# Performance work log

Measured on AMD Instinct MI355X. Metric: run time of the kernel, lower is better.

The kernel has to match this reference:

```python
import jax, jax.numpy as jnp
import numpy as np

N = 200_000      # nodes
E = 6_400_000    # edges (avg degree 32)
G = 2_000        # graphs
SD = 10          # state_dim
ROUNDS = 3


def setup_inputs() -> dict:
    key = jax.random.key(0)
    ks = jax.random.split(key, 10)
    node_coordinates = jax.random.normal(ks[0], (N, 3), dtype=jnp.float32)
    node_graph_index = jnp.sort(jax.random.randint(ks[1], (N,), 0, G))
    node_from = jax.random.randint(ks[2], (E,), 0, N)
    node_to = jax.random.randint(ks[3], (E,), 0, N)
    edge_lengths = jax.random.uniform(ks[4], (E, 1), dtype=jnp.float32)
    edge_vectors = jax.random.normal(ks[5], (E, 3), dtype=jnp.float32)
    # message net: Linear(14 -> 10), torch default uniform init
    lim = 1.0 / np.sqrt(SD + 4)
    W_msg = jax.random.uniform(ks[6], (SD + 4, SD), minval=-lim, maxval=lim, dtype=jnp.float32)
    b_msg = jax.random.uniform(ks[7], (SD,), minval=-lim, maxval=lim, dtype=jnp.float32)
    # output net: Linear(10 -> 4), xavier_normal weight, default bias
    W_out = jax.random.normal(ks[8], (SD, 4), dtype=jnp.float32) * np.float32(np.sqrt(2.0 / (SD + 4)))
    lim_o = 1.0 / np.sqrt(SD)
    b_out = jax.random.uniform(ks[9], (4,), minval=-lim_o, maxval=lim_o, dtype=jnp.float32)
    return dict(node_coordinates=node_coordinates, edge_lengths=edge_lengths,
                edge_vectors=edge_vectors, W_msg=W_msg, b_msg=b_msg,
                W_out=W_out, b_out=b_out, node_from=node_from, node_to=node_to,
                node_graph_index=node_graph_index, num_nodes=N, num_graphs=G)


def reference(node_coordinates, edge_lengths, edge_vectors, W_msg, b_msg,
              W_out, b_out, node_from, node_to, node_graph_index,
              num_nodes, num_graphs):
    c_from = node_coordinates[node_from]                      # (E,3) gather
    c_to = node_coordinates[node_to]                          # (E,3) gather
    coord_sum = jnp.sum(jnp.abs(c_from), axis=1, keepdims=True)       # (E,1)
    dot1 = jnp.sum(c_from * c_to, axis=1, keepdims=True)              # (E,1)
    dot2 = jnp.sum(c_from * edge_vectors, axis=1, keepdims=True)      # (E,1)
    geo = jnp.concatenate([edge_lengths, coord_sum, dot1, dot2], axis=1)  # (E,4), identical every round

    state = jnp.zeros((num_nodes, SD), dtype=node_coordinates.dtype)
    for _ in range(ROUNDS):
        inp = jnp.concatenate([state[node_from], geo], axis=1)        # (E,14)
        msg = jnp.tanh(inp @ W_msg + b_msg)                           # (E,10)
        state = state + jax.ops.segment_sum(msg, node_to, num_segments=num_nodes)

    graph_state = jax.ops.segment_sum(state, node_graph_index, num_segments=num_graphs)  # (G,10)
    ev = graph_state @ W_out + b_out                                  # (G,4)
    gamma, v, alpha, beta = jnp.split(ev, 4, axis=1)
    sp = jax.nn.softplus
    return jnp.concatenate([gamma, sp(v), sp(alpha) + 1.0, sp(beta)], axis=1)
```

## Files before the change

kernel.cpp:

```cpp
#include <hip/hip_runtime.h>
#include <hip/hip_fp16.h>
#include <math.h>

#define SD 10
#define BSZ 64
#define EB 512
#define CTHR 1024
#define BINB 10
#define NBIN_MAX 256

typedef unsigned uvec4 __attribute__((ext_vector_type(4)));
struct rec12 { unsigned x, y, z; };
union U32H2 { unsigned u; __half2 h; };

__device__ __forceinline__ float tanh_fast(float x) {
    float e = __expf(2.0f * x);
    float r = __builtin_amdgcn_rcpf(1.0f + e);
    return 1.0f - 2.0f * r;
}

__device__ __forceinline__ float softplus_f(float x) {
    return fmaxf(x, 0.0f) + log1pf(expf(-fabsf(x)));
}


__global__ __launch_bounds__(256) void coords4_kernel(
    const float* __restrict__ coords, float4* __restrict__ coords4, int N)
{
    int n = blockIdx.x * blockDim.x + threadIdx.x;
    if (n >= N) return;
    float4 c;
    c.x = coords[n * 3 + 0];
    c.y = coords[n * 3 + 1];
    c.z = coords[n * 3 + 2];
    c.w = fabsf(c.x) + fabsf(c.y) + fabsf(c.z);
    coords4[n] = c;
}


__global__ __launch_bounds__(CTHR) void pass1_kernel(
    const float* __restrict__ elen,
    const float* __restrict__ evec,
    const int* __restrict__ nfrom,
    const int* __restrict__ nto,
    unsigned* __restrict__ s1addr,
    rec12* __restrict__ payA,
    int E, int NBIN)
{
    __shared__ unsigned hbin[NBIN_MAX];
    __shared__ unsigned curbin[NBIN_MAX];
    int b = blockIdx.x, t = threadIdx.x;
    long long ebeg = (long long)E * b / EB;
    long long eend = (long long)E * (b + 1) / EB;

    if (t < NBIN_MAX) hbin[t] = 0;
    __syncthreads();
    for (long long e = ebeg + t; e < eend; e += CTHR)
        atomicAdd(&hbin[((unsigned)__builtin_nontemporal_load(&nto[e])) >> BINB], 1u);
    __syncthreads();
    {
        unsigned v = (t < NBIN_MAX) ? hbin[t] : 0u;
        for (int d = 1; d < NBIN_MAX; d <<= 1) {
            unsigned x = (t < NBIN_MAX && t >= d) ? hbin[t - d] : 0u;
            __syncthreads();
            if (t < NBIN_MAX) hbin[t] += x;
            __syncthreads();
        }
        if (t < NBIN_MAX) curbin[t] = (unsigned)ebeg + hbin[t] - v;
    }
    __syncthreads();
    if (t < NBIN) s1addr[(size_t)t * EB + b] = curbin[t];
    if (t == 0)  s1addr[(size_t)NBIN * EB + b] = (unsigned)eend;
    __syncthreads();

    for (long long e = ebeg + t; e < eend; e += CTHR) {
        int nf = __builtin_nontemporal_load(&nfrom[e]);
        int nt = __builtin_nontemporal_load(&nto[e]);
        float l  = __builtin_nontemporal_load(&elen[e]);
        float ex = __builtin_nontemporal_load(&evec[e * 3 + 0]);
        float ey = __builtin_nontemporal_load(&evec[e * 3 + 1]);
        float ez = __builtin_nontemporal_load(&evec[e * 3 + 2]);
        unsigned bin = ((unsigned)nt) >> BINB;
        unsigned pos = atomicAdd(&curbin[bin], 1u);
        U32H2 a, c;
        a.h = __floats2half2_rn(l, ex);
        c.h = __floats2half2_rn(ey, ez);
        rec12 r;
        r.x = (unsigned)nf | (((unsigned)nt & ((1u << BINB) - 1u)) << 18);
        r.y = a.u;
        r.z = c.u;
        payA[pos] = r;
    }
}

__global__ __launch_bounds__(256) void colsum_kernel(
    const unsigned* __restrict__ s1addr, unsigned* __restrict__ binsum)
{
    __shared__ unsigned red[256];
    int q = blockIdx.x, t = threadIdx.x;
    red[t] = s1addr[(size_t)q * EB + t] + s1addr[(size_t)q * EB + t + 256];
    __syncthreads();
    for (int d = 128; d > 0; d >>= 1) {
        if (t < d) red[t] += red[t + d];
        __syncthreads();
    }
    if (t == 0) binsum[q] = red[0];
}

__global__ __launch_bounds__(256) void binstart_kernel(
    const unsigned* __restrict__ binsum, unsigned* __restrict__ binstart,
    unsigned* __restrict__ nodestart, int NBIN, int E)
{
    int t = threadIdx.x;
    unsigned b0 = binsum[0];
    for (int q = t; q <= NBIN; q += 256) binstart[q] = binsum[q] - b0;
    if (t == 0) nodestart[(size_t)NBIN << BINB] = (unsigned)E;
}

__global__ __launch_bounds__(CTHR) void pass2_kernel(
    const unsigned* __restrict__ s1addr,
    const unsigned* __restrict__ binstart,
    const float4* __restrict__ coords4,
    const rec12* __restrict__ src,
    rec12* __restrict__ dst,
    unsigned* __restrict__ nodestart,
    int NBIN)
{
    __shared__ unsigned segst[EB];
    __shared__ unsigned spref[EB + 1];
    __shared__ unsigned hist[1 << BINB];
    __shared__ unsigned cur[1 << BINB];
    int q = blockIdx.x, t = threadIdx.x;

    if (t < EB) {
        unsigned st = s1addr[(size_t)q * EB + t];
        unsigned en = s1addr[(size_t)(q + 1) * EB + t];
        segst[t] = st;
        spref[t] = en - st;
    }
    hist[t] = 0;
    __syncthreads();
    {
        unsigned v = (t < EB) ? spref[t] : 0u;
        for (int d = 1; d < EB; d <<= 1) {
            unsigned x = (t < EB && t >= d) ? spref[t - d] : 0u;
            __syncthreads();
            if (t < EB) spref[t] += x;
            __syncthreads();
        }
        unsigned incl = (t < EB) ? spref[t] : 0u;
        __syncthreads();
        if (t < EB) spref[t] = incl - v;
        if (t == EB - 1) spref[EB] = incl;
    }
    __syncthreads();
    unsigned len = spref[EB];
    unsigned obase = binstart[q];
    const unsigned* srcw = (const unsigned*)src;

    for (unsigned i = t; i < len; i += CTHR) {
        unsigned lo = 0, hi = EB;
#pragma unroll
        for (int s = 0; s < 9; s++) {
            unsigned mid = (lo + hi) >> 1;
            if (spref[mid] <= i) lo = mid; else hi = mid;
        }
        unsigned x0 = srcw[(size_t)(segst[lo] + (i - spref[lo])) * 3];
        atomicAdd(&hist[(x0 >> 18) & ((1u << BINB) - 1u)], 1u);
    }
    __syncthreads();
    unsigned hv = hist[t];
    __syncthreads();
    for (int d = 1; d < (1 << BINB); d <<= 1) {
        unsigned x = (t >= d) ? hist[t - d] : 0u;
        __syncthreads();
        hist[t] += x;
        __syncthreads();
    }
    unsigned excl = hist[t] - hv;
    cur[t] = obase + excl;
    nodestart[((size_t)q << BINB) + t] = obase + excl;
    __syncthreads();

    rec12 p0; float4 cf0;
    {
        unsigned i0 = t;
        if (i0 < len) {
            unsigned lo = 0, hi = EB;
#pragma unroll
            for (int s = 0; s < 9; s++) {
                unsigned mid = (lo + hi) >> 1;
                if (spref[mid] <= i0) lo = mid; else hi = mid;
            }
            p0 = src[segst[lo] + (i0 - spref[lo])];
            cf0 = coords4[p0.x & 0x3FFFFu];
        }
    }
    for (unsigned i = t; i < len; i += CTHR) {
        unsigned i1 = i + CTHR;
        rec12 p1 = p0; float4 cf1 = cf0;
        if (i1 < len) {
            unsigned lo = 0, hi = EB;
#pragma unroll
            for (int s = 0; s < 9; s++) {
                unsigned mid = (lo + hi) >> 1;
                if (spref[mid] <= i1) lo = mid; else hi = mid;
            }
            p1 = src[segst[lo] + (i1 - spref[lo])];
            cf1 = coords4[p1.x & 0x3FFFFu];
        }
        unsigned key = (p0.x >> 18) & ((1u << BINB) - 1u);
        unsigned pos = atomicAdd(&cur[key], 1u);
        unsigned nt = ((unsigned)q << BINB) | key;
        float4 ct = coords4[nt];
        U32H2 ya, za;
        ya.u = p0.y; za.u = p0.z;
        float g0 = __low2float(ya.h), ev0 = __high2float(ya.h);
        float ev1 = __low2float(za.h), ev2 = __high2float(za.h);
        float g2 = cf0.x * ct.x + cf0.y * ct.y + cf0.z * ct.z;
        float g3 = cf0.x * ev0 + cf0.y * ev1 + cf0.z * ev2;
        U32H2 oy, oz;
        oy.h = __floats2half2_rn(g0, cf0.w);
        oz.h = __floats2half2_rn(g2, g3);
        rec12 r;
        r.x = (p0.x & 0x3FFFFu) | ((nt & (BSZ - 1u)) << 18);
        r.y = oy.u;
        r.z = oz.u;
        dst[pos] = r;
        p0 = p1; cf0 = cf1;
    }
}


__global__ __launch_bounds__(256) void wstate_kernel(
    const float* __restrict__ state, const float* __restrict__ Wm,
    const float* __restrict__ bm, __half* __restrict__ wsth, int N)
{
    int n = blockIdx.x * blockDim.x + threadIdx.x;
    if (n >= N) return;
    const float2* sp = (const float2*)(state + (size_t)n * SD);
    float s[SD];
#pragma unroll
    for (int h = 0; h < 5; h++) { float2 v = sp[h]; s[2*h] = v.x; s[2*h+1] = v.y; }
    float t[SD];
#pragma unroll
    for (int j = 0; j < SD; j++) t[j] = bm[j];
#pragma unroll
    for (int k = 0; k < SD; k++) {
#pragma unroll
        for (int j = 0; j < SD; j++) t[j] += s[k] * Wm[k * SD + j];
    }
    unsigned* dp = (unsigned*)(wsth + (size_t)n * SD);
#pragma unroll
    for (int h = 0; h < 5; h++) {
        U32H2 cv;
        cv.h = __floats2half2_rn(t[2*h], t[2*h+1]);
        dp[h] = cv.u;
    }
}

template <bool FIRST>
__global__ __launch_bounds__(256) void round_run_kernel(
    const unsigned* __restrict__ nodestart,
    const rec12* __restrict__ payload,
    const float* __restrict__ Wm,
    const float* __restrict__ bm,
    const __half* __restrict__ wsth,
    const float* __restrict__ state_prev,
    float* __restrict__ state_next,
    int N, int E)
{
    __shared__ float acc[BSZ * SD];
    int k = blockIdx.x;
    for (int i = threadIdx.x; i < BSZ * SD; i += 256) acc[i] = 0.0f;

    int lane = threadIdx.x & 63;
    int wv = threadIdx.x >> 6;
    int grp0 = lane / 10;
    bool active = grp0 < 6;
    int grp = active ? grp0 : 5;
    int j = active ? (lane - grp0 * 10) : (lane - 60);

    float w0 = Wm[10 * SD + j];
    float w1 = Wm[11 * SD + j];
    float w2 = Wm[12 * SD + j];
    float w3 = Wm[13 * SD + j];
    float bb = bm[j];
    __syncthreads();

    unsigned beg = nodestart[(size_t)k << 6];
    unsigned end = nodestart[(size_t)(k + 1) << 6];
    unsigned len = end - beg;
    unsigned Q = (len + 3) >> 2;
    unsigned rbeg = beg + (unsigned)wv * Q;
    unsigned rend = rbeg + Q; if (rend > end) rend = end;
    unsigned eclamp = (unsigned)E - 1u;

    unsigned e0 = rbeg + (unsigned)grp;
    rec12 P0 = payload[e0 <= eclamp ? e0 : eclamp];
    unsigned e1 = e0 + 6;
    rec12 P1 = payload[e1 <= eclamp ? e1 : eclamp];
    float T0 = bb, T1 = bb;
    if (!FIRST) T0 = __half2float(wsth[(size_t)(P0.x & 0x3FFFFu) * SD + j]);

    int cur_lnt = -1;
    float accv = 0.0f;

    for (unsigned base = rbeg; base < rend; base += 6) {
        unsigned e2 = base + 12 + (unsigned)grp;
        rec12 P2 = payload[e2 <= eclamp ? e2 : eclamp];
        if (!FIRST) T1 = __half2float(wsth[(size_t)(P1.x & 0x3FFFFu) * SD + j]);
        unsigned e = base + (unsigned)grp;
        if (active && e < rend) {
            int lnt = (int)((P0.x >> 18) & (BSZ - 1));
            U32H2 c01, c23;
            c01.u = P0.y; c23.u = P0.z;
            float g0 = __low2float(c01.h), g1 = __high2float(c01.h);
            float g2 = __low2float(c23.h), g3 = __high2float(c23.h);
            float t = T0 + g0 * w0 + g1 * w1 + g2 * w2 + g3 * w3;
            if (lnt != cur_lnt) {
                if (cur_lnt >= 0) atomicAdd(&acc[cur_lnt * SD + j], accv);
                accv = 0.0f;
                cur_lnt = lnt;
            }
            accv += tanh_fast(t);
        }
        P0 = P1; P1 = P2; T0 = T1;
    }
    if (active && cur_lnt >= 0) atomicAdd(&acc[cur_lnt * SD + j], accv);
    __syncthreads();

    int base_o = k * BSZ * SD;
    int lim = N * SD - base_o;
    for (int i = threadIdx.x; i < BSZ * SD; i += 256) {
        if (i < lim) {
            float v = acc[i];
            if (!FIRST) v += state_prev[base_o + i];
            state_next[base_o + i] = v;
        }
    }
}


__global__ __launch_bounds__(256) void goff_kernel(
    const int* __restrict__ gidx, unsigned* __restrict__ goff, int N, int G)
{
    int n = blockIdx.x * blockDim.x + threadIdx.x;
    if (n >= N) return;
    int g = gidx[n];
    if (n == 0) {
        for (int q = 0; q <= g; q++) goff[q] = 0;
    } else {
        int gp = gidx[n - 1];
        for (int q = gp + 1; q <= g; q++) goff[q] = (unsigned)n;
    }
    if (n == N - 1) {
        for (int q = g + 1; q <= G; q++) goff[q] = (unsigned)N;
    }
}

__global__ __launch_bounds__(256) void gsum_kernel(
    const float* __restrict__ state, const unsigned* __restrict__ goff,
    float* __restrict__ gstate, int G)
{
    int tid = blockIdx.x * blockDim.x + threadIdx.x;
    if (tid >= G * SD * 4) return;
    int s = tid & 3;
    int rest = tid >> 2;
    int g = rest / SD;
    int j = rest - g * SD;
    unsigned beg = goff[g], end = goff[g + 1];
    unsigned len = end - beg;
    unsigned b0 = beg + (len * (unsigned)s) / 4u;
    unsigned b1 = beg + (len * (unsigned)(s + 1)) / 4u;
    float a = 0.0f;
    for (unsigned n = b0; n < b1; n++) a += state[(size_t)n * SD + j];
    atomicAdd(&gstate[(size_t)g * SD + j], a);
}

__global__ __launch_bounds__(256) void out_kernel(
    const float* __restrict__ gstate, const float* __restrict__ Wo,
    const float* __restrict__ bo, float* __restrict__ out, int G)
{
    int g = blockIdx.x * blockDim.x + threadIdx.x;
    if (g >= G) return;
    float s[SD];
#pragma unroll
    for (int k = 0; k < SD; k++) s[k] = gstate[(size_t)g * SD + k];
    float ev[4];
#pragma unroll
    for (int c = 0; c < 4; c++) {
        float a = bo[c];
#pragma unroll
        for (int k = 0; k < SD; k++) a += s[k] * Wo[k * 4 + c];
        ev[c] = a;
    }
    out[g * 4 + 0] = ev[0];
    out[g * 4 + 1] = softplus_f(ev[1]);
    out[g * 4 + 2] = softplus_f(ev[2]) + 1.0f;
    out[g * 4 + 3] = softplus_f(ev[3]);
}


template <bool FIRST>
__global__ __launch_bounds__(256) void edge_kernel_fb(
    const float* __restrict__ coords, const float* __restrict__ elen,
    const float* __restrict__ evec, const float* __restrict__ Wm,
    const float* __restrict__ bm, const int* __restrict__ nfrom,
    const int* __restrict__ nto, const float* __restrict__ state_prev,
    float* __restrict__ state_next, int E)
{
    int e = blockIdx.x * blockDim.x + threadIdx.x;
    if (e >= E) return;
    int nf = nfrom[e];
    int nt = nto[e];
    float cf0 = coords[nf*3+0], cf1 = coords[nf*3+1], cf2 = coords[nf*3+2];
    float ct0 = coords[nt*3+0], ct1 = coords[nt*3+1], ct2 = coords[nt*3+2];
    float ev0 = evec[e*3+0], ev1 = evec[e*3+1], ev2 = evec[e*3+2];
    float g0 = elen[e];
    float g1 = fabsf(cf0) + fabsf(cf1) + fabsf(cf2);
    float g2 = cf0*ct0 + cf1*ct1 + cf2*ct2;
    float g3 = cf0*ev0 + cf1*ev1 + cf2*ev2;
    float acc[SD];
#pragma unroll
    for (int j = 0; j < SD; j++) {
        acc[j] = bm[j] + g0*Wm[10*SD+j] + g1*Wm[11*SD+j] + g2*Wm[12*SD+j] + g3*Wm[13*SD+j];
    }
    if (!FIRST) {
        const float2* sp = (const float2*)(state_prev + (size_t)nf * SD);
        float s[SD];
#pragma unroll
        for (int h = 0; h < 5; h++) { float2 v = sp[h]; s[2*h] = v.x; s[2*h+1] = v.y; }
#pragma unroll
        for (int k = 0; k < SD; k++) {
#pragma unroll
            for (int j = 0; j < SD; j++) acc[j] += s[k] * Wm[k*SD+j];
        }
    }
    float* dst = state_next + (size_t)nt * SD;
#pragma unroll
    for (int j = 0; j < SD; j++) atomicAdd(dst + j, tanh_fast(acc[j]));
}

__global__ __launch_bounds__(256) void graph_reduce_fb(
    const float* __restrict__ state, const int* __restrict__ gidx,
    float* __restrict__ gstate, int N)
{
    int n = blockIdx.x * blockDim.x + threadIdx.x;
    if (n >= N) return;
    int g = gidx[n];
    const float2* sp = (const float2*)(state + (size_t)n * SD);
    float* dst = gstate + (size_t)g * SD;
#pragma unroll
    for (int h = 0; h < 5; h++) {
        float2 v = sp[h];
        atomicAdd(dst + 2*h, v.x);
        atomicAdd(dst + 2*h + 1, v.y);
    }
}


extern "C" void kernel_launch(void* const* d_in, const int* in_sizes, int n_in,
                              void* d_out, int out_size, void* d_ws, size_t ws_size,
                              hipStream_t stream) {
    const float* coords = (const float*)d_in[0];
    const float* elen   = (const float*)d_in[1];
    const float* evec   = (const float*)d_in[2];
    const float* Wm     = (const float*)d_in[3];
    const float* bm     = (const float*)d_in[4];
    const float* Wo     = (const float*)d_in[5];
    const float* bo     = (const float*)d_in[6];
    const int* nfrom    = (const int*)d_in[7];
    const int* nto      = (const int*)d_in[8];
    const int* gidx     = (const int*)d_in[9];

    const int E = in_sizes[1];
    const int N = in_sizes[9];
    const int G = out_size / 4;

    const int NBIN = (N + (1 << BINB) - 1) >> BINB;
    const int NB   = (N + BSZ - 1) / BSZ;

    const int BLK = 256;
    const int ng = (N + BLK - 1) / BLK;
    const int gg = (G + BLK - 1) / BLK;

    auto align256 = [](size_t x) { return (x + 255) & ~(size_t)255; };
    const size_t state_bytes = align256((size_t)N * SD * sizeof(float));
    const size_t wst_bytes   = align256((size_t)N * SD * sizeof(__half) + 256);
    const size_t payA_bytes  = align256((size_t)E * sizeof(rec12) + 256);
    const size_t payB_bytes  = align256((size_t)E * sizeof(rec12) + 256);
    const size_t s1a_bytes   = align256((size_t)(NBIN_MAX + 1) * EB * sizeof(unsigned));
    const size_t bsum_bytes  = align256((size_t)(NBIN_MAX + 1) * sizeof(unsigned));
    const size_t nst_bytes   = align256(((size_t)NBIN_MAX * (1 << BINB) + 2) * sizeof(unsigned));
    const size_t goff_bytes  = align256((size_t)(G + 1) * sizeof(unsigned));
    const size_t gst_bytes   = align256((size_t)G * SD * sizeof(float));
    const size_t c4_bytes    = align256((size_t)N * sizeof(float4));

    size_t o = 0;
    char* w = (char*)d_ws;
    float* stateA      = (float*)(w + o);    o += state_bytes;
    float* stateB      = (float*)(w + o);    o += state_bytes;
    __half* wsth       = (__half*)(w + o);   o += wst_bytes;
    rec12* payA        = (rec12*)(w + o);    o += payA_bytes;
    rec12* payB        = (rec12*)(w + o);    o += payB_bytes;
    unsigned* s1addr   = (unsigned*)(w + o); o += s1a_bytes;
    unsigned* binsum   = (unsigned*)(w + o); o += bsum_bytes;
    unsigned* binstart = (unsigned*)(w + o); o += bsum_bytes;
    unsigned* nodestart= (unsigned*)(w + o); o += nst_bytes;
    unsigned* goff     = (unsigned*)(w + o); o += goff_bytes;
    float* gstate      = (float*)(w + o);    o += gst_bytes;
    float4* coords4    = (float4*)(w + o);   o += c4_bytes;

    if (o <= ws_size && NBIN <= NBIN_MAX && N < (1 << 18)) {
        coords4_kernel<<<ng, BLK, 0, stream>>>(coords, coords4, N);
        pass1_kernel<<<EB, CTHR, 0, stream>>>(elen, evec, nfrom, nto,
                                              s1addr, payA, E, NBIN);
        colsum_kernel<<<NBIN + 1, 256, 0, stream>>>(s1addr, binsum);
        binstart_kernel<<<1, 256, 0, stream>>>(binsum, binstart, nodestart, NBIN, E);
        pass2_kernel<<<NBIN, CTHR, 0, stream>>>(s1addr, binstart, coords4,
                                                payA, payB, nodestart, NBIN);
        round_run_kernel<true><<<NB, BLK, 0, stream>>>(nodestart, payB, Wm, bm,
                                                       wsth, stateB, stateA, N, E);
        wstate_kernel<<<ng, BLK, 0, stream>>>(stateA, Wm, bm, wsth, N);
        round_run_kernel<false><<<NB, BLK, 0, stream>>>(nodestart, payB, Wm, bm,
                                                        wsth, stateA, stateB, N, E);
        wstate_kernel<<<ng, BLK, 0, stream>>>(stateB, Wm, bm, wsth, N);
        round_run_kernel<false><<<NB, BLK, 0, stream>>>(nodestart, payB, Wm, bm,
                                                        wsth, stateB, stateA, N, E);
        hipMemsetAsync(gstate, 0, (size_t)G * SD * sizeof(float), stream);
        goff_kernel<<<ng, BLK, 0, stream>>>(gidx, goff, N, G);
        gsum_kernel<<<(G * SD * 4 + BLK - 1) / BLK, BLK, 0, stream>>>(stateA, goff, gstate, G);
        out_kernel<<<gg, BLK, 0, stream>>>(gstate, Wo, bo, (float*)d_out, G);
    } else {
        const int eg = (E + BLK - 1) / BLK;
        float* gstateF = (float*)(w + 2 * state_bytes);
        hipMemsetAsync(stateA, 0, state_bytes, stream);
        hipMemsetAsync(gstateF, 0, (size_t)G * SD * sizeof(float), stream);
        edge_kernel_fb<true><<<eg, BLK, 0, stream>>>(coords, elen, evec, Wm, bm,
                                                     nfrom, nto, stateA, stateA, E);
        hipMemcpyAsync(stateB, stateA, state_bytes, hipMemcpyDeviceToDevice, stream);
        edge_kernel_fb<false><<<eg, BLK, 0, stream>>>(coords, elen, evec, Wm, bm,
                                                      nfrom, nto, stateA, stateB, E);
        hipMemcpyAsync(stateA, stateB, state_bytes, hipMemcpyDeviceToDevice, stream);
        edge_kernel_fb<false><<<eg, BLK, 0, stream>>>(coords, elen, evec, Wm, bm,
                                                      nfrom, nto, stateB, stateA, E);
        graph_reduce_fb<<<ng, BLK, 0, stream>>>(stateA, gidx, gstateF, N);
        out_kernel<<<gg, BLK, 0, stream>>>(gstateF, Wo, bo, (float*)d_out, G);
    }
}
```

Before: 702.3 us.

## Stage pass2 scatter through LDS per key half-range for coalesced output writes

Bins are reduced from 10 to 9 bits, so each bin covers fewer nodes and more bins exist. Pass2 now sweeps the input once per half of the key range and scatters matching records into a large shared-memory staging buffer (about 130 KB of LDS). It then computes the geometry features and writes the output contiguously instead of scattering each record to global memory. The cost is re-reading the bin's input once per key half, a large LDS footprint that limits occupancy, and an unstaged fallback path when a half-range overflows the buffer.

```diff
diff --git a/kernel.cpp b/kernel.cpp
--- a/kernel.cpp
+++ b/kernel.cpp
@@ -6,8 +6,10 @@
 #define BSZ 64
 #define EB 512
 #define CTHR 1024
-#define BINB 10
-#define NBIN_MAX 256
+#define BINB 9
+#define NBIN_MAX 512
+#define HSZ 256
+#define SCAP 10880
 
 typedef unsigned uvec4 __attribute__((ext_vector_type(4)));
 struct rec12 { unsigned x, y, z; };
@@ -130,7 +132,9 @@
     __shared__ unsigned spref[EB + 1];
     __shared__ unsigned hist[1 << BINB];
     __shared__ unsigned cur[1 << BINB];
+    __shared__ rec12 stage[SCAP];
     int q = blockIdx.x, t = threadIdx.x;
+    const unsigned KMASK = (1u << BINB) - 1u;
 
     if (t < EB) {
         unsigned st = s1addr[(size_t)q * EB + t];
@@ -138,7 +142,7 @@
         segst[t] = st;
         spref[t] = en - st;
     }
-    hist[t] = 0;
+    if (t < (1 << BINB)) hist[t] = 0;
     __syncthreads();
     {
         unsigned v = (t < EB) ? spref[t] : 0u;
@@ -166,68 +170,114 @@
             if (spref[mid] <= i) lo = mid; else hi = mid;
         }
         unsigned x0 = srcw[(size_t)(segst[lo] + (i - spref[lo])) * 3];
-        atomicAdd(&hist[(x0 >> 18) & ((1u << BINB) - 1u)], 1u);
-    }
-    __syncthreads();
-    unsigned hv = hist[t];
+        atomicAdd(&hist[(x0 >> 18) & KMASK], 1u);
+    }
+    __syncthreads();
+    unsigned hv = (t < (1 << BINB)) ? hist[t] : 0u;
     __syncthreads();
     for (int d = 1; d < (1 << BINB); d <<= 1) {
-        unsigned x = (t >= d) ? hist[t - d] : 0u;
+        unsigned x = (t < (1 << BINB) && t >= d) ? hist[t - d] : 0u;
         __syncthreads();
-        hist[t] += x;
+        if (t < (1 << BINB)) hist[t] += x;
         __syncthreads();
     }
-    unsigned excl = hist[t] - hv;
-    cur[t] = obase + excl;
-    nodestart[((size_t)q << BINB) + t] = obase + excl;
-    __syncthreads();
-
-    rec12 p0; float4 cf0;
-    {
-        unsigned i0 = t;
-        if (i0 < len) {
-            unsigned lo = 0, hi = EB;
-#pragma unroll
-            for (int s = 0; s < 9; s++) {
-                unsigned mid = (lo + hi) >> 1;
-                if (spref[mid] <= i0) lo = mid; else hi = mid;
+    if (t < (1 << BINB)) {
+        unsigned excl = hist[t] - hv;
+        cur[t] = obase + excl;
+        nodestart[((size_t)q << BINB) + t] = obase + excl;
+    }
+    __syncthreads();
+
+    for (int h = 0; h < (1 << BINB) / HSZ; ++h) {
+        unsigned kbeg = (unsigned)h * HSZ, kend = kbeg + HSZ;
+        unsigned qs = kbeg ? hist[kbeg - 1] : 0u;
+        unsigned qe = hist[kend - 1];
+        unsigned qlen = qe - qs;
+        unsigned qg = obase + qs;
+        if (qlen <= (unsigned)SCAP) {
+            for (unsigned i = t; i < len; i += CTHR) {
+                unsigned lo = 0, hi = EB;
+#pragma unroll
+                for (int s = 0; s < 9; s++) {
+                    unsigned mid = (lo + hi) >> 1;
+                    if (spref[mid] <= i) lo = mid; else hi = mid;
+                }
+                rec12 p = src[segst[lo] + (i - spref[lo])];
+                unsigned key = (p.x >> 18) & KMASK;
+                if (key >= kbeg && key < kend) {
+                    unsigned pos = atomicAdd(&cur[key], 1u);
+                    stage[pos - qg] = p;
+                }
             }
-            p0 = src[segst[lo] + (i0 - spref[lo])];
-            cf0 = coords4[p0.x & 0x3FFFFu];
+            __syncthreads();
+            unsigned i = t;
+            rec12 p0; float4 cf0;
+            if (i < qlen) {
+                p0 = stage[i];
+                cf0 = coords4[p0.x & 0x3FFFFu];
+            }
+            while (i < qlen) {
+                unsigned i1 = i + CTHR;
+                rec12 p1 = p0; float4 cf1 = cf0;
+                if (i1 < qlen) {
+                    p1 = stage[i1];
+                    cf1 = coords4[p1.x & 0x3FFFFu];
+                }
+                unsigned key = (p0.x >> 18) & KMASK;
+                unsigned nf = p0.x & 0x3FFFFu;
+                unsigned nt = ((unsigned)q << BINB) | key;
+                float4 ct = coords4[nt];
+                U32H2 ya, za;
+                ya.u = p0.y; za.u = p0.z;
+                float g0 = __low2float(ya.h), ev0 = __high2float(ya.h);
+                float ev1 = __low2float(za.h), ev2 = __high2float(za.h);
+                float g2 = cf0.x * ct.x + cf0.y * ct.y + cf0.z * ct.z;
+                float g3 = cf0.x * ev0 + cf0.y * ev1 + cf0.z * ev2;
+                U32H2 oy, oz;
+                oy.h = __floats2half2_rn(g0, cf0.w);
+                oz.h = __floats2half2_rn(g2, g3);
+                rec12 r;
+                r.x = nf | ((nt & (BSZ - 1u)) << 18);
+                r.y = oy.u;
+                r.z = oz.u;
+                dst[qg + i] = r;
+                i = i1; p0 = p1; cf0 = cf1;
+            }
+            __syncthreads();
+        } else {
+            for (unsigned i = t; i < len; i += CTHR) {
+                unsigned lo = 0, hi = EB;
+#pragma unroll
+                for (int s = 0; s < 9; s++) {
+                    unsigned mid = (lo + hi) >> 1;
+                    if (spref[mid] <= i) lo = mid; else hi = mid;
+                }
+                rec12 p = src[segst[lo] + (i - spref[lo])];
+                unsigned key = (p.x >> 18) & KMASK;
+                if (key >= kbeg && key < kend) {
+                    unsigned pos = atomicAdd(&cur[key], 1u);
+                    unsigned nf = p.x & 0x3FFFFu;
+                    unsigned nt = ((unsigned)q << BINB) | key;
+                    float4 cf = coords4[nf];
+                    float4 ct = coords4[nt];
+                    U32H2 ya, za;
+                    ya.u = p.y; za.u = p.z;
+                    float g0 = __low2float(ya.h), ev0 = __high2float(ya.h);
+                    float ev1 = __low2float(za.h), ev2 = __high2float(za.h);
+                    float g2 = cf.x * ct.x + cf.y * ct.y + cf.z * ct.z;
+                    float g3 = cf.x * ev0 + cf.y * ev1 + cf.z * ev2;
+                    U32H2 oy, oz;
+                    oy.h = __floats2half2_rn(g0, cf.w);
+                    oz.h = __floats2half2_rn(g2, g3);
+                    rec12 r;
+                    r.x = nf | ((nt & (BSZ - 1u)) << 18);
+                    r.y = oy.u;
+                    r.z = oz.u;
+                    dst[pos] = r;
+                }
+            }
+            __syncthreads();
         }
-    }
-    for (unsigned i = t; i < len; i += CTHR) {
-        unsigned i1 = i + CTHR;
-        rec12 p1 = p0; float4 cf1 = cf0;
-        if (i1 < len) {
-            unsigned lo = 0, hi = EB;
-#pragma unroll
-            for (int s = 0; s < 9; s++) {
-                unsigned mid = (lo + hi) >> 1;
-                if (spref[mid] <= i1) lo = mid; else hi = mid;
-            }
-            p1 = src[segst[lo] + (i1 - spref[lo])];
-            cf1 = coords4[p1.x & 0x3FFFFu];
-        }
-        unsigned key = (p0.x >> 18) & ((1u << BINB) - 1u);
-        unsigned pos = atomicAdd(&cur[key], 1u);
-        unsigned nt = ((unsigned)q << BINB) | key;
-        float4 ct = coords4[nt];
-        U32H2 ya, za;
-        ya.u = p0.y; za.u = p0.z;
-        float g0 = __low2float(ya.h), ev0 = __high2float(ya.h);
-        float ev1 = __low2float(za.h), ev2 = __high2float(za.h);
-        float g2 = cf0.x * ct.x + cf0.y * ct.y + cf0.z * ct.z;
-        float g3 = cf0.x * ev0 + cf0.y * ev1 + cf0.z * ev2;
-        U32H2 oy, oz;
-        oy.h = __floats2half2_rn(g0, cf0.w);
-        oz.h = __floats2half2_rn(g2, g3);
-        rec12 r;
-        r.x = (p0.x & 0x3FFFFu) | ((nt & (BSZ - 1u)) << 18);
-        r.y = oy.u;
-        r.z = oz.u;
-        dst[pos] = r;
-        p0 = p1; cf0 = cf1;
     }
 }
 
```

New measurement: 680.0 us. 3.2% less time.
